# Kernel tuning notes

Measured on AMD Instinct MI355X. Metric: run time of the kernel, lower is better.

The kernel has to match this reference:

```python
import jax, jax.numpy as jnp
import numpy as np

_EPS = 1e-5

def _bn(x, g, t, m, v):
    # inference-mode BatchNorm (channels-last)
    return g * (x - m) * jax.lax.rsqrt(v + _EPS) + t

def _lin(x, w, b):
    # 1x1 conv == linear over last (channel) axis; w: (out, in)
    return jnp.einsum('...c,oc->...o', x, w) + b

def _forward(points, k, c0_w, c0_b, c0_g, c0_t, c0_m, c0_v,
             c1_w, c1_b, c1_g, c1_t, c1_m, c1_v,
             a0_w, a0_b, a0_g, a0_t, a0_m, a0_v,
             a1_w, a1_b, a1_g, a1_t, a1_m, a1_v,
             a2_w, a2_b, a2_g, a2_t, a2_m, a2_v,
             c2_w, c2_b, c2_g, c2_t, c2_m, c2_v,
             c3_w, c3_b, c3_g, c3_t, c3_m, c3_v,
             c4_w, c4_b):
    B, N, _ = points.shape
    # per-point MLP: 3 -> 64 -> 64
    x = jax.nn.relu(_bn(_lin(points, c0_w, c0_b), c0_g, c0_t, c0_m, c0_v))
    x = jax.nn.relu(_bn(_lin(x, c1_w, c1_b), c1_g, c1_t, c1_m, c1_v))
    # kNN via squared distances (same ordering as cdist); idx: (B,N,k)
    sq = jnp.sum(points * points, axis=-1)  # (B,N)
    d = sq[:, :, None] + sq[:, None, :] - 2.0 * jnp.einsum('bnc,bmc->bnm', points, points)
    idx = jax.lax.top_k(-d, k)[1]  # (B,N,k) smallest distances
    bidx = jnp.arange(B)[:, None, None]
    grouped_xyz = points[bidx, idx] - points[:, :, None, :]  # (B,N,k,3), centered
    grouped_pts = x[bidx, idx]                                # (B,N,k,64)
    g = jnp.concatenate([grouped_xyz, grouped_pts], axis=-1)  # (B,N,k,67)
    # per-neighbor MLP 67 -> 64 -> 128 -> 128
    for (w, b, ga, t, m, v) in ((a0_w, a0_b, a0_g, a0_t, a0_m, a0_v),
                                (a1_w, a1_b, a1_g, a1_t, a1_m, a1_v),
                                (a2_w, a2_b, a2_g, a2_t, a2_m, a2_v)):
        g = jax.nn.relu(_bn(_lin(g, w, b), ga, t, m, v))
    local = jnp.max(g, axis=2)                 # (B,N,128) max over k neighbors
    gf = jnp.max(local, axis=1, keepdims=True)  # (B,1,128) global feature
    feat = jnp.concatenate([local, jnp.broadcast_to(gf, local.shape)], axis=-1)  # (B,N,256)
    feat = jax.nn.relu(_bn(_lin(feat, c2_w, c2_b), c2_g, c2_t, c2_m, c2_v))
    feat = jax.nn.relu(_bn(_lin(feat, c3_w, c3_b), c3_g, c3_t, c3_m, c3_v))
    # dropout is identity in eval mode
    return _lin(feat, c4_w, c4_b)  # (B,N,6)

def setup_inputs() -> dict:
    key = jax.random.key(0)
    B, N, K = 8, 4096, 16
    specs = [("c0", 64, 3, True), ("c1", 64, 64, True), ("a0", 64, 67, True),
             ("a1", 128, 64, True), ("a2", 128, 128, True), ("c2", 256, 256, True),
             ("c3", 128, 256, True), ("c4", 6, 128, False)]
    inp = {"points": jax.random.normal(key, (B, N, 3), jnp.float32)}
    i = 0
    for name, o, c, has_bn in specs:
        i += 1
        kw = jax.random.fold_in(key, i)
        inp[name + "_w"] = jax.random.normal(kw, (o, c), jnp.float32) * 0.05
        inp[name + "_b"] = jnp.zeros((o,), jnp.float32)
        if has_bn:
            inp[name + "_g"] = jnp.ones((o,), jnp.float32)
            inp[name + "_t"] = jnp.zeros((o,), jnp.float32)
            inp[name + "_m"] = jax.random.normal(jax.random.fold_in(kw, 1), (o,), jnp.float32) * 0.05
            inp[name + "_v"] = jnp.ones((o,), jnp.float32)
    inp["k"] = K
    return inp

def reference(points, c0_w, c0_b, c0_g, c0_t, c0_m, c0_v,
              c1_w, c1_b, c1_g, c1_t, c1_m, c1_v,
              a0_w, a0_b, a0_g, a0_t, a0_m, a0_v,
              a1_w, a1_b, a1_g, a1_t, a1_m, a1_v,
              a2_w, a2_b, a2_g, a2_t, a2_m, a2_v,
              c2_w, c2_b, c2_g, c2_t, c2_m, c2_v,
              c3_w, c3_b, c3_g, c3_t, c3_m, c3_v,
              c4_w, c4_b, k):
    return _forward(points, k, c0_w, c0_b, c0_g, c0_t, c0_m, c0_v,
                    c1_w, c1_b, c1_g, c1_t, c1_m, c1_v,
                    a0_w, a0_b, a0_g, a0_t, a0_m, a0_v,
                    a1_w, a1_b, a1_g, a1_t, a1_m, a1_v,
                    a2_w, a2_b, a2_g, a2_t, a2_m, a2_v,
                    c2_w, c2_b, c2_g, c2_t, c2_m, c2_v,
                    c3_w, c3_b, c3_g, c3_t, c3_m, c3_v,
                    c4_w, c4_b)
```

## Files before the change

### kernel.cpp

```cpp
#include <hip/hip_runtime.h>
#include <math.h>


#define EPSBN 1e-5f

typedef _Float16 v8h  __attribute__((ext_vector_type(8)));
typedef _Float16 v4h  __attribute__((ext_vector_type(4)));
typedef float    v16f __attribute__((ext_vector_type(16)));

#define W0T_OFF   0
#define B0_OFF    192
#define W1T_OFF   256
#define B1_OFF    4352
#define A0XT_OFF  4416
#define A0FT_OFF  4608
#define BA0_OFF   8704
#define A1T_OFF   8768
#define BA1_OFF   16960
#define A2T_OFF   17088
#define BA2_OFF   33472
#define C2T_OFF   33600
#define C3H_OFF   66368
#define BC2_OFF   99136
#define BC3_OFF   132160
#define C4T_OFF   132288
#define BC4_OFF   133056
#define PTS4_OFF  133120
#define Q_OFF     264192
#define C_OFF     2361344
#define IDX_OFF   4458496
#define LOCAL_OFF 4982784
#define GF_OFF    9177088

__device__ __forceinline__ void fold_one(int e, const float* w, const float* b,
    const float* g, const float* t, const float* m, const float* v,
    float* wt, float* bo, int O, int Cfull, int cbeg)
{
    int o = e % O, c = e / O;
    float s = 1.0f;
    if (g) s = g[o] * (1.0f / sqrtf(v[o] + EPSBN));
    wt[c * O + o] = w[o * Cfull + cbeg + c] * s;
    if (c == 0 && bo) {
        float bias = b[o];
        if (g) bias = (bias - m[o]) * s + t[o];
        bo[o] = bias;
    }
}

__global__ __launch_bounds__(256) void fold_kernel(
    const float* c0w, const float* c0b, const float* c0g, const float* c0t, const float* c0m, const float* c0v,
    const float* c1w, const float* c1b, const float* c1g, const float* c1t, const float* c1m, const float* c1v,
    const float* a0w, const float* a0b, const float* a0g, const float* a0t, const float* a0m, const float* a0v,
    const float* a1w, const float* a1b, const float* a1g, const float* a1t, const float* a1m, const float* a1v,
    const float* a2w, const float* a2b, const float* a2g, const float* a2t, const float* a2m, const float* a2v,
    const float* c2w, const float* c2b, const float* c2g, const float* c2t, const float* c2m, const float* c2v,
    const float* c3w, const float* c3b, const float* c3g, const float* c3t, const float* c3m, const float* c3v,
    const float* c4w, const float* c4b,
    float* ws)
{
    int e = blockIdx.x * 256 + threadIdx.x;
    if (e < 192)        { fold_one(e,          c0w, c0b, c0g, c0t, c0m, c0v, ws + W0T_OFF,  ws + B0_OFF,  64, 3,   0); return; }
    e -= 192;
    if (e < 4096)       { fold_one(e,          c1w, c1b, c1g, c1t, c1m, c1v, ws + W1T_OFF,  ws + B1_OFF,  64, 64,  0); return; }
    e -= 4096;
    if (e < 192)        { fold_one(e,          a0w, a0b, a0g, a0t, a0m, a0v, ws + A0XT_OFF, ws + BA0_OFF, 64, 67,  0); return; }
    e -= 192;
    if (e < 4096)       { fold_one(e,          a0w, a0b, a0g, a0t, a0m, a0v, ws + A0FT_OFF, nullptr,      64, 67,  3); return; }
    e -= 4096;
    if (e < 8192) {
        int j = e & 7, l = (e >> 3) & 63, kf = (e >> 9) & 3, wv = e >> 11;
        int o = wv * 32 + (l & 31);
        int c = kf * 16 + (l >> 5) * 8 + j;
        float s = a1g[o] * (1.0f / sqrtf(a1v[o] + EPSBN));
        ((_Float16*)(ws + A1T_OFF))[e] = (_Float16)(a1w[o * 64 + c] * s);
        if (c == 0) ws[BA1_OFF + o] = (a1b[o] - a1m[o]) * s + a1t[o];
        return;
    }
    e -= 8192;
    if (e < 16384) {
        int j = e & 7, l = (e >> 3) & 63, kf = (e >> 9) & 7, wv = e >> 12;
        int o = wv * 32 + (l & 31);
        int c = kf * 16 + (l >> 5) * 8 + j;
        float s = a2g[o] * (1.0f / sqrtf(a2v[o] + EPSBN));
        ((_Float16*)(ws + A2T_OFF))[e] = (_Float16)(a2w[o * 128 + c] * s);
        if (c == 0) ws[BA2_OFF + o] = (a2b[o] - a2m[o]) * s + a2t[o];
        return;
    }
    e -= 16384;
    if (e < 65536) {
        int j = e & 7, l = (e >> 3) & 63, s5 = (e >> 9) & 15, ot = e >> 13;
        int o = ot * 32 + (l & 31);
        int c = s5 * 16 + (l >> 5) * 8 + j;
        float sc = c2g[o] * (1.0f / sqrtf(c2v[o] + EPSBN));
        ((_Float16*)(ws + C2T_OFF))[e] = (_Float16)(c2w[o * 256 + c] * sc);
        if (c == 0) ws[BC2_OFF + o] = (c2b[o] - c2m[o]) * sc + c2t[o];
        return;
    }
    e -= 65536;
    if (e < 32768) {
        int j = e & 7, l = (e >> 3) & 63, s5 = (e >> 9) & 15, ot = e >> 13;
        int o = ot * 32 + (l & 31);
        int c = s5 * 16 + (l >> 5) * 8 + j;
        float sc = c3g[o] * (1.0f / sqrtf(c3v[o] + EPSBN));
        ((_Float16*)(ws + C3H_OFF))[e] = (_Float16)(c3w[o * 256 + c] * sc);
        if (c == 0) ws[BC3_OFF + o] = (c3b[o] - c3m[o]) * sc + c3t[o];
        return;
    }
    e -= 32768;
    if (e < 768)        { fold_one(e,          c4w, c4b, nullptr, nullptr, nullptr, nullptr, ws + C4T_OFF, ws + BC4_OFF, 6, 128, 0); return; }
    e -= 768;
    if (e < 1024)       { ws[GF_OFF + e] = 0.0f; return; }
}

__global__ __launch_bounds__(256) void point_mlp_kernel(const float* __restrict__ pts, float* __restrict__ ws)
{
    __shared__ float sh[4][64][4];
    __shared__ float sx[4][64][4];
    int lane = threadIdx.x & 63;
    int wv = threadIdx.x >> 6;
    int pid0 = blockIdx.x * 16 + wv * 4;

    const float* pc = pts + (size_t)pid0 * 3;
    float c0x = pc[0], c0y = pc[1],  c0z = pc[2];
    float c1x = pc[3], c1y = pc[4],  c1z = pc[5];
    float c2x = pc[6], c2y = pc[7],  c2z = pc[8];
    float c3x = pc[9], c3y = pc[10], c3z = pc[11];

    if (lane < 4) {
        const float* pp = pts + (size_t)(pid0 + lane) * 3;
        float xx = pp[0], yy = pp[1], zz = pp[2];
        float sq = __fadd_rn(__fadd_rn(__fmul_rn(xx, xx), __fmul_rn(yy, yy)), __fmul_rn(zz, zz));
        ((float4*)(ws + PTS4_OFF))[pid0 + lane] = make_float4(xx, yy, zz, sq);
    }

    const float* W0T  = ws + W0T_OFF;
    const float* B0   = ws + B0_OFF;
    const float* W1T  = ws + W1T_OFF;
    const float* B1   = ws + B1_OFF;
    const float* A0XT = ws + A0XT_OFF;
    const float* A0FT = ws + A0FT_OFF;
    const float* BA0  = ws + BA0_OFF;

    float b0 = B0[lane];
    float w0a = W0T[lane], w0b = W0T[64 + lane], w0c = W0T[128 + lane];
    float4 h;
    h.x = fmaxf(fmaf(c0z, w0c, fmaf(c0y, w0b, fmaf(c0x, w0a, b0))), 0.0f);
    h.y = fmaxf(fmaf(c1z, w0c, fmaf(c1y, w0b, fmaf(c1x, w0a, b0))), 0.0f);
    h.z = fmaxf(fmaf(c2z, w0c, fmaf(c2y, w0b, fmaf(c2x, w0a, b0))), 0.0f);
    h.w = fmaxf(fmaf(c3z, w0c, fmaf(c3y, w0b, fmaf(c3x, w0a, b0))), 0.0f);
    *(float4*)&sh[wv][lane][0] = h;

    float b1v = B1[lane];
    float a0 = b1v, a1 = b1v, a2 = b1v, a3 = b1v;
    #pragma unroll 8
    for (int c = 0; c < 64; ++c) {
        float w = W1T[c * 64 + lane];
        float4 hv = *(const float4*)&sh[wv][c][0];
        a0 = fmaf(w, hv.x, a0);
        a1 = fmaf(w, hv.y, a1);
        a2 = fmaf(w, hv.z, a2);
        a3 = fmaf(w, hv.w, a3);
    }
    float4 xv;
    xv.x = fmaxf(a0, 0.0f);
    xv.y = fmaxf(a1, 0.0f);
    xv.z = fmaxf(a2, 0.0f);
    xv.w = fmaxf(a3, 0.0f);
    *(float4*)&sx[wv][lane][0] = xv;

    float ax = A0XT[lane], ay = A0XT[64 + lane], az = A0XT[128 + lane];
    float q0 = __fmul_rn(c0x, ax); q0 = fmaf(c0y, ay, q0); q0 = fmaf(c0z, az, q0);
    float q1 = __fmul_rn(c1x, ax); q1 = fmaf(c1y, ay, q1); q1 = fmaf(c1z, az, q1);
    float q2 = __fmul_rn(c2x, ax); q2 = fmaf(c2y, ay, q2); q2 = fmaf(c2z, az, q2);
    float q3 = __fmul_rn(c3x, ax); q3 = fmaf(c3y, ay, q3); q3 = fmaf(c3z, az, q3);
    ws[Q_OFF + (size_t)(pid0 + 0) * 64 + lane] = q0;
    ws[Q_OFF + (size_t)(pid0 + 1) * 64 + lane] = q1;
    ws[Q_OFF + (size_t)(pid0 + 2) * 64 + lane] = q2;
    ws[Q_OFF + (size_t)(pid0 + 3) * 64 + lane] = q3;

    float ba = BA0[lane];
    float e0 = q0 + ba, e1 = q1 + ba, e2 = q2 + ba, e3 = q3 + ba;
    #pragma unroll 8
    for (int c = 0; c < 64; ++c) {
        float w = A0FT[c * 64 + lane];
        float4 sv = *(const float4*)&sx[wv][c][0];
        e0 = fmaf(w, sv.x, e0);
        e1 = fmaf(w, sv.y, e1);
        e2 = fmaf(w, sv.z, e2);
        e3 = fmaf(w, sv.w, e3);
    }
    ws[C_OFF + (size_t)(pid0 + 0) * 64 + lane] = e0;
    ws[C_OFF + (size_t)(pid0 + 1) * 64 + lane] = e1;
    ws[C_OFF + (size_t)(pid0 + 2) * 64 + lane] = e2;
    ws[C_OFF + (size_t)(pid0 + 3) * 64 + lane] = e3;
}

__device__ __forceinline__ float dist2_ref(float xn, float yn, float zn, float sqn, float4 pm)
{
    float dot = __fmul_rn(xn, pm.x);
    dot = __fmaf_rn(yn, pm.y, dot);
    dot = __fmaf_rn(zn, pm.z, dot);
    float s = __fadd_rn(sqn, pm.w);
    return __fmaf_rn(-2.0f, dot, s);
}

#define KNN_CAP 64
__global__ __launch_bounds__(1024) void knn_kernel(float* __restrict__ ws)
{
    __shared__ float gmins[64 * 65];
    __shared__ float bufd[16][72];
    __shared__ int   bufi[16][72];
    __shared__ int   cnt[64];

    const float4* __restrict__ pts4 = (const float4*)(ws + PTS4_OFF);
    int* IDX = (int*)(ws + IDX_OFF);

    const int l     = threadIdx.x & 63;
    const int row   = l;
    const int wvu   = __builtin_amdgcn_readfirstlane(threadIdx.x >> 6);
    const int base  = (blockIdx.x >> 6) << 12;
    const int rbase = blockIdx.x * 64;
    const int r     = rbase + row;

    float4 pn = pts4[r];
    float xn = pn.x, yn = pn.y, zn = pn.z, sqn = pn.w;

    #pragma unroll
    for (int g = 0; g < 4; ++g) {
        const float4* __restrict__ cp = pts4 + base + wvu * 256 + g * 64;
        float mn0 = INFINITY, mn1 = INFINITY, mn2 = INFINITY, mn3 = INFINITY;
        #pragma unroll 4
        for (int i = 0; i < 64; i += 4) {
            mn0 = fminf(mn0, dist2_ref(xn, yn, zn, sqn, cp[i + 0]));
            mn1 = fminf(mn1, dist2_ref(xn, yn, zn, sqn, cp[i + 1]));
            mn2 = fminf(mn2, dist2_ref(xn, yn, zn, sqn, cp[i + 2]));
            mn3 = fminf(mn3, dist2_ref(xn, yn, zn, sqn, cp[i + 3]));
        }
        gmins[row * 65 + wvu * 4 + g] = fminf(fminf(mn0, mn1), fminf(mn2, mn3));
    }
    __syncthreads();

    for (int rr = 0; rr < 4; ++rr) {
        int rw = wvu * 4 + rr;
        float gm = gmins[rw * 65 + l];

        float v = gm;
        #pragma unroll
        for (int k = 2; k <= 64; k <<= 1) {
            #pragma unroll
            for (int j = k >> 1; j > 0; j >>= 1) {
                float o = __shfl_xor(v, j);
                bool mx = (((l & j) != 0) == ((l & k) == 0));
                v = mx ? fmaxf(v, o) : fminf(v, o);
            }
        }
        float tv = __shfl(v, 16);

        unsigned long long qm = __ballot(gm <= tv);

        float4 pr = pts4[rbase + rw];
        float xr = pr.x, yr = pr.y, zr = pr.z, sr = pr.w;

        int cr = 0;
        #define KNN_PROC(GG, CV)                                                   \
        {                                                                          \
            float d = dist2_ref(xr, yr, zr, sr, (CV));                             \
            bool p = (d <= tv);                                                    \
            unsigned long long mk = __ballot(p);                                   \
            int my = __builtin_amdgcn_mbcnt_hi((unsigned)(mk >> 32),               \
                     __builtin_amdgcn_mbcnt_lo((unsigned)mk, 0));                  \
            int slot = cr + my;                                                    \
            if (p && slot < KNN_CAP) { bufd[wvu][slot] = d; bufi[wvu][slot] = (GG) * 64 + l; } \
            cr += (int)__popcll(mk);                                               \
        }
        while (qm) {
            int g0 = __ffsll((unsigned long long)qm) - 1; qm &= qm - 1;
            int g1 = -1, g2 = -1, g3 = -1;
            if (qm) { g1 = __ffsll((unsigned long long)qm) - 1; qm &= qm - 1;
                if (qm) { g2 = __ffsll((unsigned long long)qm) - 1; qm &= qm - 1;
                    if (qm) { g3 = __ffsll((unsigned long long)qm) - 1; qm &= qm - 1; } } }
            float4 cv0 = pts4[base + g0 * 64 + l];
            float4 cv1, cv2, cv3;
            if (g1 >= 0) cv1 = pts4[base + g1 * 64 + l];
            if (g2 >= 0) cv2 = pts4[base + g2 * 64 + l];
            if (g3 >= 0) cv3 = pts4[base + g3 * 64 + l];
            KNN_PROC(g0, cv0);
            if (g1 >= 0) KNN_PROC(g1, cv1);
            if (g2 >= 0) KNN_PROC(g2, cv2);
            if (g3 >= 0) KNN_PROC(g3, cv3);
        }
        #undef KNN_PROC
        if (l == 0) cnt[rw] = cr;

        if (cr <= KNN_CAP) {
            unsigned long long key = ~0ULL;
            if (l < cr) {
                unsigned u = __float_as_uint(bufd[wvu][l]);
                u = (u & 0x80000000u) ? ~u : (u | 0x80000000u);
                key = ((unsigned long long)u << 32) | (unsigned)bufi[wvu][l];
            }
            #pragma unroll
            for (int k = 2; k <= 64; k <<= 1) {
                #pragma unroll
                for (int j = k >> 1; j > 0; j >>= 1) {
                    unsigned long long o = __shfl_xor(key, j);
                    bool mx = (((l & j) != 0) == ((l & k) == 0));
                    key = mx ? (key > o ? key : o) : (key < o ? key : o);
                }
            }
            if (l < 16)
                IDX[(rbase + rw) * 16 + l] = (int)(key & 0xFFFFFFFFu);
        }
    }
    __syncthreads();

    if (threadIdx.x < 64 && cnt[threadIdx.x] > KNN_CAP) {
        int* out = IDX + (rbase + threadIdx.x) * 16;
        float hd[16]; int hi[16];
        #pragma unroll
        for (int t2 = 0; t2 < 16; ++t2) { hd[t2] = INFINITY; hi[t2] = 0; }
        for (int mm = 0; mm < 4096; ++mm) {
            float d = dist2_ref(xn, yn, zn, sqn, pts4[base + mm]);
            if (d < hd[15]) {
                float vd = d; int vi = mm;
                #pragma unroll
                for (int t2 = 0; t2 < 16; ++t2) {
                    bool sm = vd < hd[t2];
                    float td = hd[t2]; int ti = hi[t2];
                    if (sm) { hd[t2] = vd; hi[t2] = vi; vd = td; vi = ti; }
                }
            }
        }
        for (int jj = 0; jj < 16; ++jj) out[jj] = hi[jj];
    }
}

__device__ __forceinline__ float max16_dpp(float v)
{
    int vi = __float_as_int(v);
    v = fmaxf(v, __int_as_float(__builtin_amdgcn_update_dpp(0, vi, 0xB1, 0xf, 0xf, true)));
    vi = __float_as_int(v);
    v = fmaxf(v, __int_as_float(__builtin_amdgcn_update_dpp(0, vi, 0x4E, 0xf, 0xf, true)));
    vi = __float_as_int(v);
    v = fmaxf(v, __int_as_float(__builtin_amdgcn_update_dpp(0, vi, 0x141, 0xf, 0xf, true)));
    vi = __float_as_int(v);
    v = fmaxf(v, __int_as_float(__builtin_amdgcn_update_dpp(0, vi, 0x140, 0xf, 0xf, true)));
    return v;
}

__device__ __forceinline__ void nbr_stage_g1(
    _Float16* sG1, const float* Cf, const float* Qf,
    int t, int gpt0, int g, int base, int m)
{
    int r = t >> 2, cs = t & 3;
    int gpt = gpt0 + g * 4 + (r >> 4);
    const float4* crow = (const float4*)(Cf + (size_t)(base + m) * 64) + cs * 4;
    const float4* qrow = (const float4*)(Qf + (size_t)gpt * 64) + cs * 4;
    v8h h0, h1;
    #pragma unroll
    for (int u = 0; u < 2; ++u) {
        float4 cv = crow[u], qv = qrow[u];
        h0[u * 4 + 0] = (_Float16)fmaxf(cv.x - qv.x, 0.0f);
        h0[u * 4 + 1] = (_Float16)fmaxf(cv.y - qv.y, 0.0f);
        h0[u * 4 + 2] = (_Float16)fmaxf(cv.z - qv.z, 0.0f);
        h0[u * 4 + 3] = (_Float16)fmaxf(cv.w - qv.w, 0.0f);
    }
    #pragma unroll
    for (int u = 0; u < 2; ++u) {
        float4 cv = crow[2 + u], qv = qrow[2 + u];
        h1[u * 4 + 0] = (_Float16)fmaxf(cv.x - qv.x, 0.0f);
        h1[u * 4 + 1] = (_Float16)fmaxf(cv.y - qv.y, 0.0f);
        h1[u * 4 + 2] = (_Float16)fmaxf(cv.z - qv.z, 0.0f);
        h1[u * 4 + 3] = (_Float16)fmaxf(cv.w - qv.w, 0.0f);
    }
    int rs = r & 7;
    *(v8h*)&sG1[r * 64 + ((cs * 2    ) ^ rs) * 8] = h0;
    *(v8h*)&sG1[r * 64 + ((cs * 2 + 1) ^ rs) * 8] = h1;
}

__global__ __launch_bounds__(256) void nbr_mlp_mfma_kernel(float* __restrict__ ws)
{
    __shared__ __align__(16) unsigned char smem[33792];
    _Float16* sG1   = (_Float16*)smem;
    _Float16* sH1   = (_Float16*)(smem + 8192);
    float*    sPool = (float*)(smem + 24576);
    float*    sB1   = (float*)(smem + 32768);
    float*    sB2   = (float*)(smem + 33280);

    const int t   = threadIdx.x;
    const int l   = t & 63;
    const int w   = t >> 6;
    const int ln  = l & 31;
    const int hi  = l >> 5;
    const int blk = blockIdx.x;
    const int gpt0 = blk * 16;
    const int base = (blk >> 8) << 12;

    const float* Cf = ws + C_OFF;
    const float* Qf = ws + Q_OFF;
    const int* IDX = (const int*)(ws + IDX_OFF);

    if (t < 128) sB1[t] = ws[BA1_OFF + t];
    else         sB2[t - 128] = ws[BA2_OFF + (t - 128)];

    int mi[4];
    {
        int r = t >> 2;
        #pragma unroll
        for (int g = 0; g < 4; ++g)
            mi[g] = IDX[(gpt0 + g * 4 + (r >> 4)) * 16 + (r & 15)];
    }

    v8h fa[4], fa2[8];
    {
        const float4* a1img = (const float4*)(ws + A1T_OFF);
        const float4* a2img = (const float4*)(ws + A2T_OFF);
        #pragma unroll
        for (int kf = 0; kf < 4; ++kf) {
            float4 tmp = a1img[(w * 4 + kf) * 64 + l];
            fa[kf] = *(v8h*)&tmp;
        }
        #pragma unroll
        for (int kf = 0; kf < 8; ++kf) {
            float4 tmp = a2img[(w * 8 + kf) * 64 + l];
            fa2[kf] = *(v8h*)&tmp;
        }
    }

    nbr_stage_g1(sG1, Cf, Qf, t, gpt0, 0, base, mi[0]);
    __syncthreads();

    for (int g = 0; g < 4; ++g) {
        #pragma unroll
        for (int rt = 0; rt < 2; ++rt) {
            int r = rt * 32 + ln, rs = r & 7;
            v16f acc;
            #pragma unroll
            for (int i = 0; i < 16; ++i) acc[i] = 0.0f;
            #pragma unroll
            for (int kf = 0; kf < 4; ++kf) {
                v8h fb = *(const v8h*)&sG1[r * 64 + ((kf * 2 + hi) ^ rs) * 8];
                acc = __builtin_amdgcn_mfma_f32_32x32x16_f16(fa[kf], fb, acc, 0, 0, 0);
            }
            #pragma unroll
            for (int q = 0; q < 4; ++q) {
                float4 b4 = *(const float4*)&sB1[w * 32 + 8 * q + 4 * hi];
                v4h hv;
                hv[0] = (_Float16)fmaxf(acc[q * 4 + 0] + b4.x, 0.0f);
                hv[1] = (_Float16)fmaxf(acc[q * 4 + 1] + b4.y, 0.0f);
                hv[2] = (_Float16)fmaxf(acc[q * 4 + 2] + b4.z, 0.0f);
                hv[3] = (_Float16)fmaxf(acc[q * 4 + 3] + b4.w, 0.0f);
                int gg = w * 4 + q;
                *(v4h*)&sH1[r * 128 + ((gg ^ rs) * 8) + 4 * hi] = hv;
            }
        }
        __syncthreads();

        if (g < 3) nbr_stage_g1(sG1, Cf, Qf, t, gpt0, g + 1, base, mi[g + 1]);

        #pragma unroll
        for (int rt = 0; rt < 2; ++rt) {
            int r = rt * 32 + ln, rs = r & 7;
            v16f acc;
            #pragma unroll
            for (int i = 0; i < 16; ++i) acc[i] = 0.0f;
            #pragma unroll
            for (int kf = 0; kf < 8; ++kf) {
                v8h fb = *(const v8h*)&sH1[r * 128 + ((kf * 2 + hi) ^ rs) * 8];
                acc = __builtin_amdgcn_mfma_f32_32x32x16_f16(fa2[kf], fb, acc, 0, 0, 0);
            }
            #pragma unroll
            for (int i = 0; i < 16; ++i) acc[i] = max16_dpp(acc[i]);
            if ((l & 15) == 0) {
                int p = g * 4 + rt * 2 + ((l >> 4) & 1);
                #pragma unroll
                for (int q = 0; q < 4; ++q) {
                    float4 b4 = *(const float4*)&sB2[w * 32 + 8 * q + 4 * hi];
                    float4 o4;
                    o4.x = fmaxf(acc[q * 4 + 0] + b4.x, 0.0f);
                    o4.y = fmaxf(acc[q * 4 + 1] + b4.y, 0.0f);
                    o4.z = fmaxf(acc[q * 4 + 2] + b4.z, 0.0f);
                    o4.w = fmaxf(acc[q * 4 + 3] + b4.w, 0.0f);
                    int ob = w * 32 + 8 * q + 4 * hi;
                    *(float4*)&sPool[p * 128 + ob] = o4;
                }
            }
        }
        __syncthreads();
    }

    {
        float* LOCAL = ws + LOCAL_OFF;
        const float4* sp4 = (const float4*)sPool;
        #pragma unroll
        for (int u = 0; u < 2; ++u) {
            int e = t + 256 * u;
            int pp = e >> 5, cc = e & 31;
            ((float4*)&LOCAL[(size_t)(gpt0 + pp) * 128])[cc] = sp4[e];
        }
    }

    if (t < 128) {
        float m = 0.0f;
        #pragma unroll
        for (int p = 0; p < 16; ++p) m = fmaxf(m, sPool[p * 128 + t]);
        atomicMax((int*)(ws + GF_OFF) + (blk >> 8) * 128 + t, __float_as_int(m));
    }
}

__global__ __launch_bounds__(256) void head_mfma_kernel(float* __restrict__ ws, float* __restrict__ out)
{
    __shared__ __align__(16) unsigned char smem[66560];
    _Float16* sF  = (_Float16*)smem;
    float*    sF3 = (float*)smem;
    _Float16* sF2 = (_Float16*)(smem + 33792);

    const int t  = threadIdx.x;
    const int l  = t & 63;
    const int w  = t >> 6;
    const int ln = l & 31;
    const int hi = l >> 5;
    const int gpt0 = blockIdx.x * 64;
    const int b = blockIdx.x >> 6;

    const float4* c2h = (const float4*)(ws + C2T_OFF);
    const float4* c3h = (const float4*)(ws + C3H_OFF);

    {
        int m = t >> 2, cs = t & 3;
        const float4* src = (cs < 2)
            ? (const float4*)(ws + LOCAL_OFF + (size_t)(gpt0 + m) * 128) + cs * 16
            : (const float4*)(ws + GF_OFF + b * 128) + (cs - 2) * 16;
        int c0 = cs * 64;
        #pragma unroll
        for (int u = 0; u < 8; ++u) {
            float4 a0 = src[u * 2], a1 = src[u * 2 + 1];
            v8h h;
            h[0] = (_Float16)a0.x; h[1] = (_Float16)a0.y;
            h[2] = (_Float16)a0.z; h[3] = (_Float16)a0.w;
            h[4] = (_Float16)a1.x; h[5] = (_Float16)a1.y;
            h[6] = (_Float16)a1.z; h[7] = (_Float16)a1.w;
            int g = ((c0 >> 3) + u) ^ (m & 31);
            *(v8h*)&sF[m * 256 + g * 8] = h;
        }
    }
    __syncthreads();

    #pragma unroll
    for (int ot = 0; ot < 2; ++ot) {
        int ot2 = 2 * w + ot;
        v8h fa[16];
        #pragma unroll
        for (int s = 0; s < 16; ++s) {
            float4 tmp = c2h[(ot2 * 16 + s) * 64 + l];
            fa[s] = *(v8h*)&tmp;
        }
        float b2[16];
        #pragma unroll
        for (int i = 0; i < 16; ++i)
            b2[i] = ws[BC2_OFF + ot2 * 32 + (i & 3) + 8 * (i >> 2) + 4 * hi];
        #pragma unroll
        for (int mt = 0; mt < 2; ++mt) {
            int m = mt * 32 + ln;
            v16f acc;
            #pragma unroll
            for (int i = 0; i < 16; ++i) acc[i] = 0.0f;
            #pragma unroll
            for (int s = 0; s < 16; ++s) {
                v8h fb = *(const v8h*)&sF[m * 256 + (((2 * s + hi) ^ ln) * 8)];
                acc = __builtin_amdgcn_mfma_f32_32x32x16_f16(fa[s], fb, acc, 0, 0, 0);
            }
            #pragma unroll
            for (int q = 0; q < 4; ++q) {
                v4h hv;
                #pragma unroll
                for (int j = 0; j < 4; ++j)
                    hv[j] = (_Float16)fmaxf(acc[q * 4 + j] + b2[q * 4 + j], 0.0f);
                *(v4h*)&sF2[m * 256 + (((ot2 * 4 + q) ^ ln) * 8) + 4 * hi] = hv;
            }
        }
    }
    __syncthreads();

    {
        v8h fa[16];
        #pragma unroll
        for (int s = 0; s < 16; ++s) {
            float4 tmp = c3h[(w * 16 + s) * 64 + l];
            fa[s] = *(v8h*)&tmp;
        }
        float b3[16];
        #pragma unroll
        for (int i = 0; i < 16; ++i)
            b3[i] = ws[BC3_OFF + w * 32 + (i & 3) + 8 * (i >> 2) + 4 * hi];
        #pragma unroll
        for (int mt = 0; mt < 2; ++mt) {
            int m = mt * 32 + ln;
            v16f acc;
            #pragma unroll
            for (int i = 0; i < 16; ++i) acc[i] = 0.0f;
            #pragma unroll
            for (int s = 0; s < 16; ++s) {
                v8h fb = *(const v8h*)&sF2[m * 256 + (((2 * s + hi) ^ ln) * 8)];
                acc = __builtin_amdgcn_mfma_f32_32x32x16_f16(fa[s], fb, acc, 0, 0, 0);
            }
            #pragma unroll
            for (int q = 0; q < 4; ++q) {
                float4 hv;
                hv.x = fmaxf(acc[q * 4 + 0] + b3[q * 4 + 0], 0.0f);
                hv.y = fmaxf(acc[q * 4 + 1] + b3[q * 4 + 1], 0.0f);
                hv.z = fmaxf(acc[q * 4 + 2] + b3[q * 4 + 2], 0.0f);
                hv.w = fmaxf(acc[q * 4 + 3] + b3[q * 4 + 3], 0.0f);
                *(float4*)&sF3[m * 132 + w * 32 + q * 8 + 4 * hi] = hv;
            }
        }
    }
    __syncthreads();

    const float* C4T = ws + C4T_OFF;
    for (int mo = t; mo < 384; mo += 256) {
        int m = mo / 6, o = mo - m * 6;
        float a = ws[BC4_OFF + o];
        const float4* f4 = (const float4*)(sF3 + m * 132);
        #pragma unroll 8
        for (int kq = 0; kq < 32; ++kq) {
            float4 f = f4[kq];
            a = fmaf(f.x, C4T[(kq * 4 + 0) * 6 + o], a);
            a = fmaf(f.y, C4T[(kq * 4 + 1) * 6 + o], a);
            a = fmaf(f.z, C4T[(kq * 4 + 2) * 6 + o], a);
            a = fmaf(f.w, C4T[(kq * 4 + 3) * 6 + o], a);
        }
        out[(size_t)(gpt0 + m) * 6 + o] = a;
    }
}

extern "C" void kernel_launch(void* const* d_in, const int* in_sizes, int n_in,
                              void* d_out, int out_size, void* d_ws, size_t ws_size,
                              hipStream_t stream)
{
    const float* pts = (const float*)d_in[0];
    float* ws = (float*)d_ws;
    float* out = (float*)d_out;

    fold_kernel<<<521, 256, 0, stream>>>(
        (const float*)d_in[1],  (const float*)d_in[2],  (const float*)d_in[3],  (const float*)d_in[4],  (const float*)d_in[5],  (const float*)d_in[6],
        (const float*)d_in[7],  (const float*)d_in[8],  (const float*)d_in[9],  (const float*)d_in[10], (const float*)d_in[11], (const float*)d_in[12],
        (const float*)d_in[13], (const float*)d_in[14], (const float*)d_in[15], (const float*)d_in[16], (const float*)d_in[17], (const float*)d_in[18],
        (const float*)d_in[19], (const float*)d_in[20], (const float*)d_in[21], (const float*)d_in[22], (const float*)d_in[23], (const float*)d_in[24],
        (const float*)d_in[25], (const float*)d_in[26], (const float*)d_in[27], (const float*)d_in[28], (const float*)d_in[29], (const float*)d_in[30],
        (const float*)d_in[31], (const float*)d_in[32], (const float*)d_in[33], (const float*)d_in[34], (const float*)d_in[35], (const float*)d_in[36],
        (const float*)d_in[37], (const float*)d_in[38], (const float*)d_in[39], (const float*)d_in[40], (const float*)d_in[41], (const float*)d_in[42],
        (const float*)d_in[43], (const float*)d_in[44],
        ws);

    point_mlp_kernel<<<2048, 256, 0, stream>>>(pts, ws);
    knn_kernel<<<512, 1024, 0, stream>>>(ws);
    nbr_mlp_mfma_kernel<<<2048, 256, 0, stream>>>(ws);
    head_mfma_kernel<<<512, 256, 0, stream>>>(ws, out);
}
```

Baseline: 318.5 us.

## Drop per-row norm from kNN group-min pass and batch four row bitonic sorts

The first pass of the kNN kernel now computes a reduced distance that leaves out the constant query-norm term, so each candidate costs one fewer add. A small margin is added to the threshold to absorb rounding differences between the reduced and the full distance. The four per-row bitonic threshold sorts are interleaved to raise instruction-level parallelism, and the final key sort uses a shorter 32-wide network when at most 32 candidates survive. The margin can admit more candidates, which raises the chance of hitting the slow fallback path.

```diff
diff --git a/kernel.cpp b/kernel.cpp
--- a/kernel.cpp
+++ b/kernel.cpp
@@ -204,101 +204,77 @@
     return __fmaf_rn(-2.0f, dot, s);
 }
 
+__device__ __forceinline__ float dtilde(float xn, float yn, float zn, float4 pm)
+{
+    float dot = __fmul_rn(xn, pm.x);
+    dot = __fmaf_rn(yn, pm.y, dot);
+    dot = __fmaf_rn(zn, pm.z, dot);
+    return __fmaf_rn(-2.0f, dot, pm.w);
+}
+
 #define KNN_CAP 64
-__global__ __launch_bounds__(1024) void knn_kernel(float* __restrict__ ws)
-{
-    __shared__ float gmins[64 * 65];
-    __shared__ float bufd[16][72];
-    __shared__ int   bufi[16][72];
-    __shared__ int   cnt[64];
-
-    const float4* __restrict__ pts4 = (const float4*)(ws + PTS4_OFF);
-    int* IDX = (int*)(ws + IDX_OFF);
-
-    const int l     = threadIdx.x & 63;
-    const int row   = l;
-    const int wvu   = __builtin_amdgcn_readfirstlane(threadIdx.x >> 6);
-    const int base  = (blockIdx.x >> 6) << 12;
-    const int rbase = blockIdx.x * 64;
-    const int r     = rbase + row;
-
-    float4 pn = pts4[r];
-    float xn = pn.x, yn = pn.y, zn = pn.z, sqn = pn.w;
-
-    #pragma unroll
-    for (int g = 0; g < 4; ++g) {
-        const float4* __restrict__ cp = pts4 + base + wvu * 256 + g * 64;
-        float mn0 = INFINITY, mn1 = INFINITY, mn2 = INFINITY, mn3 = INFINITY;
-        #pragma unroll 4
-        for (int i = 0; i < 64; i += 4) {
-            mn0 = fminf(mn0, dist2_ref(xn, yn, zn, sqn, cp[i + 0]));
-            mn1 = fminf(mn1, dist2_ref(xn, yn, zn, sqn, cp[i + 1]));
-            mn2 = fminf(mn2, dist2_ref(xn, yn, zn, sqn, cp[i + 2]));
-            mn3 = fminf(mn3, dist2_ref(xn, yn, zn, sqn, cp[i + 3]));
-        }
-        gmins[row * 65 + wvu * 4 + g] = fminf(fminf(mn0, mn1), fminf(mn2, mn3));
-    }
-    __syncthreads();
-
-    for (int rr = 0; rr < 4; ++rr) {
-        int rw = wvu * 4 + rr;
-        float gm = gmins[rw * 65 + l];
-
-        float v = gm;
-        #pragma unroll
-        for (int k = 2; k <= 64; k <<= 1) {
-            #pragma unroll
-            for (int j = k >> 1; j > 0; j >>= 1) {
-                float o = __shfl_xor(v, j);
-                bool mx = (((l & j) != 0) == ((l & k) == 0));
-                v = mx ? fmaxf(v, o) : fminf(v, o);
-            }
-        }
-        float tv = __shfl(v, 16);
-
-        unsigned long long qm = __ballot(gm <= tv);
-
-        float4 pr = pts4[rbase + rw];
-        float xr = pr.x, yr = pr.y, zr = pr.z, sr = pr.w;
-
-        int cr = 0;
-        #define KNN_PROC(GG, CV)                                                   \
-        {                                                                          \
-            float d = dist2_ref(xr, yr, zr, sr, (CV));                             \
-            bool p = (d <= tv);                                                    \
-            unsigned long long mk = __ballot(p);                                   \
-            int my = __builtin_amdgcn_mbcnt_hi((unsigned)(mk >> 32),               \
-                     __builtin_amdgcn_mbcnt_lo((unsigned)mk, 0));                  \
-            int slot = cr + my;                                                    \
-            if (p && slot < KNN_CAP) { bufd[wvu][slot] = d; bufi[wvu][slot] = (GG) * 64 + l; } \
-            cr += (int)__popcll(mk);                                               \
-        }
-        while (qm) {
-            int g0 = __ffsll((unsigned long long)qm) - 1; qm &= qm - 1;
-            int g1 = -1, g2 = -1, g3 = -1;
-            if (qm) { g1 = __ffsll((unsigned long long)qm) - 1; qm &= qm - 1;
-                if (qm) { g2 = __ffsll((unsigned long long)qm) - 1; qm &= qm - 1;
-                    if (qm) { g3 = __ffsll((unsigned long long)qm) - 1; qm &= qm - 1; } } }
-            float4 cv0 = pts4[base + g0 * 64 + l];
-            float4 cv1, cv2, cv3;
-            if (g1 >= 0) cv1 = pts4[base + g1 * 64 + l];
-            if (g2 >= 0) cv2 = pts4[base + g2 * 64 + l];
-            if (g3 >= 0) cv3 = pts4[base + g3 * 64 + l];
-            KNN_PROC(g0, cv0);
-            if (g1 >= 0) KNN_PROC(g1, cv1);
-            if (g2 >= 0) KNN_PROC(g2, cv2);
-            if (g3 >= 0) KNN_PROC(g3, cv3);
-        }
-        #undef KNN_PROC
-        if (l == 0) cnt[rw] = cr;
-
-        if (cr <= KNN_CAP) {
-            unsigned long long key = ~0ULL;
-            if (l < cr) {
-                unsigned u = __float_as_uint(bufd[wvu][l]);
-                u = (u & 0x80000000u) ? ~u : (u | 0x80000000u);
-                key = ((unsigned long long)u << 32) | (unsigned)bufi[wvu][l];
-            }
+#define KNN_MARGIN 1e-3f
+
+__device__ __forceinline__ void knn_row(
+    const float4* __restrict__ pts4, int* __restrict__ IDX,
+    float* __restrict__ bufdW, int* __restrict__ bufiW, int* __restrict__ cntp,
+    int base, int rbase, int rw, int l, float gm, float tvd)
+{
+    unsigned long long qm = __ballot(gm <= tvd);
+
+    float4 pr = pts4[rbase + rw];
+    float xr = pr.x, yr = pr.y, zr = pr.z, sr = pr.w;
+    float tve = __fadd_rn(sr, tvd);
+
+    int cr = 0;
+    #define KNN_PROC(GG, CV)                                                   \
+    {                                                                          \
+        float d = dist2_ref(xr, yr, zr, sr, (CV));                             \
+        bool p = (d <= tve);                                                   \
+        unsigned long long mk = __ballot(p);                                   \
+        int my = __builtin_amdgcn_mbcnt_hi((unsigned)(mk >> 32),               \
+                 __builtin_amdgcn_mbcnt_lo((unsigned)mk, 0));                  \
+        int slot = cr + my;                                                    \
+        if (p && slot < KNN_CAP) { bufdW[slot] = d; bufiW[slot] = (GG) * 64 + l; } \
+        cr += (int)__popcll(mk);                                               \
+    }
+    while (qm) {
+        int g0 = __ffsll((unsigned long long)qm) - 1; qm &= qm - 1;
+        int g1 = -1, g2 = -1, g3 = -1;
+        if (qm) { g1 = __ffsll((unsigned long long)qm) - 1; qm &= qm - 1;
+            if (qm) { g2 = __ffsll((unsigned long long)qm) - 1; qm &= qm - 1;
+                if (qm) { g3 = __ffsll((unsigned long long)qm) - 1; qm &= qm - 1; } } }
+        float4 cv0 = pts4[base + g0 * 64 + l];
+        float4 cv1, cv2, cv3;
+        if (g1 >= 0) cv1 = pts4[base + g1 * 64 + l];
+        if (g2 >= 0) cv2 = pts4[base + g2 * 64 + l];
+        if (g3 >= 0) cv3 = pts4[base + g3 * 64 + l];
+        KNN_PROC(g0, cv0);
+        if (g1 >= 0) KNN_PROC(g1, cv1);
+        if (g2 >= 0) KNN_PROC(g2, cv2);
+        if (g3 >= 0) KNN_PROC(g3, cv3);
+    }
+    #undef KNN_PROC
+    if (l == 0) *cntp = cr;
+
+    if (cr <= KNN_CAP) {
+        unsigned long long key = ~0ULL;
+        if (l < cr) {
+            unsigned u = __float_as_uint(bufdW[l]);
+            u = (u & 0x80000000u) ? ~u : (u | 0x80000000u);
+            key = ((unsigned long long)u << 32) | (unsigned)bufiW[l];
+        }
+        if (cr <= 32) {
+            #pragma unroll
+            for (int k = 2; k <= 32; k <<= 1) {
+                #pragma unroll
+                for (int j = k >> 1; j > 0; j >>= 1) {
+                    unsigned long long o = __shfl_xor(key, j);
+                    bool mx = (((l & j) != 0) == ((l & k) == 0));
+                    key = mx ? (key > o ? key : o) : (key < o ? key : o);
+                }
+            }
+        } else {
             #pragma unroll
             for (int k = 2; k <= 64; k <<= 1) {
                 #pragma unroll
@@ -308,10 +284,77 @@
                     key = mx ? (key > o ? key : o) : (key < o ? key : o);
                 }
             }
-            if (l < 16)
-                IDX[(rbase + rw) * 16 + l] = (int)(key & 0xFFFFFFFFu);
-        }
-    }
+        }
+        if (l < 16)
+            IDX[(rbase + rw) * 16 + l] = (int)(key & 0xFFFFFFFFu);
+    }
+}
+
+__global__ __launch_bounds__(1024) void knn_kernel(float* __restrict__ ws)
+{
+    __shared__ float gmins[64 * 65];
+    __shared__ float bufd[16][72];
+    __shared__ int   bufi[16][72];
+    __shared__ int   cnt[64];
+
+    const float4* __restrict__ pts4 = (const float4*)(ws + PTS4_OFF);
+    int* IDX = (int*)(ws + IDX_OFF);
+
+    const int l     = threadIdx.x & 63;
+    const int row   = l;
+    const int wvu   = __builtin_amdgcn_readfirstlane(threadIdx.x >> 6);
+    const int base  = (blockIdx.x >> 6) << 12;
+    const int rbase = blockIdx.x * 64;
+    const int r     = rbase + row;
+
+    float4 pn = pts4[r];
+    float xn = pn.x, yn = pn.y, zn = pn.z, sqn = pn.w;
+    (void)sqn;
+
+    #pragma unroll
+    for (int g = 0; g < 4; ++g) {
+        const float4* __restrict__ cp = pts4 + base + wvu * 256 + g * 64;
+        float mn0 = INFINITY, mn1 = INFINITY, mn2 = INFINITY, mn3 = INFINITY;
+        #pragma unroll 4
+        for (int i = 0; i < 64; i += 4) {
+            mn0 = fminf(mn0, dtilde(xn, yn, zn, cp[i + 0]));
+            mn1 = fminf(mn1, dtilde(xn, yn, zn, cp[i + 1]));
+            mn2 = fminf(mn2, dtilde(xn, yn, zn, cp[i + 2]));
+            mn3 = fminf(mn3, dtilde(xn, yn, zn, cp[i + 3]));
+        }
+        gmins[row * 65 + wvu * 4 + g] = fminf(fminf(mn0, mn1), fminf(mn2, mn3));
+    }
+    __syncthreads();
+
+    float gm0 = gmins[(wvu * 4 + 0) * 65 + l];
+    float gm1 = gmins[(wvu * 4 + 1) * 65 + l];
+    float gm2 = gmins[(wvu * 4 + 2) * 65 + l];
+    float gm3 = gmins[(wvu * 4 + 3) * 65 + l];
+    float v0 = gm0, v1 = gm1, v2 = gm2, v3 = gm3;
+    #pragma unroll
+    for (int k = 2; k <= 64; k <<= 1) {
+        #pragma unroll
+        for (int j = k >> 1; j > 0; j >>= 1) {
+            float o0 = __shfl_xor(v0, j);
+            float o1 = __shfl_xor(v1, j);
+            float o2 = __shfl_xor(v2, j);
+            float o3 = __shfl_xor(v3, j);
+            bool mx = (((l & j) != 0) == ((l & k) == 0));
+            v0 = mx ? fmaxf(v0, o0) : fminf(v0, o0);
+            v1 = mx ? fmaxf(v1, o1) : fminf(v1, o1);
+            v2 = mx ? fmaxf(v2, o2) : fminf(v2, o2);
+            v3 = mx ? fmaxf(v3, o3) : fminf(v3, o3);
+        }
+    }
+    float tvd0 = __shfl(v0, 16) + KNN_MARGIN;
+    float tvd1 = __shfl(v1, 16) + KNN_MARGIN;
+    float tvd2 = __shfl(v2, 16) + KNN_MARGIN;
+    float tvd3 = __shfl(v3, 16) + KNN_MARGIN;
+
+    knn_row(pts4, IDX, bufd[wvu], bufi[wvu], &cnt[wvu * 4 + 0], base, rbase, wvu * 4 + 0, l, gm0, tvd0);
+    knn_row(pts4, IDX, bufd[wvu], bufi[wvu], &cnt[wvu * 4 + 1], base, rbase, wvu * 4 + 1, l, gm1, tvd1);
+    knn_row(pts4, IDX, bufd[wvu], bufi[wvu], &cnt[wvu * 4 + 2], base, rbase, wvu * 4 + 2, l, gm2, tvd2);
+    knn_row(pts4, IDX, bufd[wvu], bufi[wvu], &cnt[wvu * 4 + 3], base, rbase, wvu * 4 + 3, l, gm3, tvd3);
     __syncthreads();
 
     if (threadIdx.x < 64 && cnt[threadIdx.x] > KNN_CAP) {
@@ -320,7 +363,7 @@
         #pragma unroll
         for (int t2 = 0; t2 < 16; ++t2) { hd[t2] = INFINITY; hi[t2] = 0; }
         for (int mm = 0; mm < 4096; ++mm) {
-            float d = dist2_ref(xn, yn, zn, sqn, pts4[base + mm]);
+            float d = dist2_ref(xn, yn, zn, pn.w, pts4[base + mm]);
             if (d < hd[15]) {
                 float vd = d; int vi = mm;
                 #pragma unroll
```

After: 312.0 us. 1.02x faster.
